# Kernel tuning notes

Measured on AMD Instinct MI355X. Metric: run time of the kernel, lower is better.

## Reference

```python
import jax, jax.numpy as jnp
import numpy as np

N = 100_000      # nodes (10kb Hi-C bins)
E = 3_200_000    # edges (avg degree 32)
IN = 6           # histone-mark features
HID1 = 6
HID2 = 30
HEADS = 4
NEG_SLOPE = 0.2  # PyG GATConv default LeakyReLU slope


def setup_inputs() -> dict:
    key = jax.random.key(0)
    ks = jax.random.split(key, 16)
    def glorot(k, shape, fan_in):
        return (jax.random.normal(k, shape, jnp.float32) / np.float32(np.sqrt(fan_in)))
    x = jax.random.normal(ks[0], (N, IN), jnp.float32)
    edge_index = jax.random.randint(ks[1], (2, E), 0, N, dtype=jnp.int32)
    edge_attr = jax.random.uniform(ks[2], (E,), jnp.float32)  # ignored (edge_dim=None)
    # GATConv 1: IN -> HID1, HEADS, concat=True
    w1 = glorot(ks[3], (IN, HEADS * HID1), IN)
    att_src1 = glorot(ks[4], (HEADS, HID1), HID1)
    att_dst1 = glorot(ks[5], (HEADS, HID1), HID1)
    b1 = jnp.zeros((HEADS * HID1,), jnp.float32)
    # GATConv 2: HEADS*HID1 -> HID2, HEADS, concat=False (head mean)
    w2 = glorot(ks[6], (HEADS * HID1, HEADS * HID2), HEADS * HID1)
    att_src2 = glorot(ks[7], (HEADS, HID2), HID2)
    att_dst2 = glorot(ks[8], (HEADS, HID2), HID2)
    b2 = jnp.zeros((HID2,), jnp.float32)
    # MLP head
    ffw1 = glorot(ks[9], (HID2, HID2 // 2), HID2)
    ffb1 = jnp.zeros((HID2 // 2,), jnp.float32)
    ffw2 = glorot(ks[10], (HID2 // 2, 2), HID2 // 2)
    ffb2 = jnp.zeros((2,), jnp.float32)
    return {"x": x, "edge_index": edge_index, "edge_attr": edge_attr,
            "w1": w1, "att_src1": att_src1, "att_dst1": att_dst1, "b1": b1,
            "w2": w2, "att_src2": att_src2, "att_dst2": att_dst2, "b2": b2,
            "ffw1": ffw1, "ffb1": ffb1, "ffw2": ffw2, "ffb2": ffb2}


def _leaky(z):
    return jnp.where(z > 0, z, NEG_SLOPE * z)


def _gat_conv(x, src, dst, W, a_src, a_dst, b, heads, ch, concat):
    n = x.shape[0]
    h = (x @ W).reshape(n, heads, ch)                       # [N,H,C]
    asrc = jnp.einsum('nhc,hc->nh', h, a_src)               # [N,H]
    adst = jnp.einsum('nhc,hc->nh', h, a_dst)               # [N,H]
    e = _leaky(asrc[src] + adst[dst])                       # [E,H]
    # stable segment softmax over incoming edges of each dst node
    m = jax.ops.segment_max(e, dst, num_segments=n)
    e = jnp.exp(e - m[dst])
    denom = jax.ops.segment_sum(e, dst, num_segments=n)
    alpha = e / (denom[dst] + 1e-16)                        # [E,H]
    msg = h[src] * alpha[:, :, None]                        # [E,H,C]
    out = jax.ops.segment_sum(msg, dst, num_segments=n)     # [N,H,C]
    out = out.reshape(n, heads * ch) if concat else out.mean(axis=1)
    return out + b


def reference(x, edge_index, edge_attr, w1, att_src1, att_dst1, b1,
              w2, att_src2, att_dst2, b2, ffw1, ffb1, ffw2, ffb2):
    n = x.shape[0]
    # PyG GATConv add_self_loops=True (edge_attr ignored: edge_dim=None)
    loops = jnp.arange(n, dtype=edge_index.dtype)
    ei = jnp.concatenate([edge_index, jnp.stack([loops, loops])], axis=1)
    src, dst = ei[0], ei[1]
    h = jax.nn.relu(_gat_conv(x, src, dst, w1, att_src1, att_dst1, b1, HEADS, HID1, True))
    h = jax.nn.relu(_gat_conv(h, src, dst, w2, att_src2, att_dst2, b2, HEADS, HID2, False))
    # dropout(p=0.5) is identity at inference
    h = jax.nn.relu(h @ ffw1 + ffb1)
    return h @ ffw2 + ffb2
```

## Files before the change

### kernel.cpp

```cpp
#include <hip/hip_runtime.h>
#include <hip/hip_fp16.h>

#define NEG_SLOPE 0.2f
#define NPB 128
#define MAXB 1024

__global__ void p0_count(const int* __restrict__ dst, int* __restrict__ bcnt,
                         int E, int nbuck)
{
    __shared__ int hist[MAXB];
    for (int b = threadIdx.x; b < nbuck; b += blockDim.x) hist[b] = 0;
    __syncthreads();
    int tile = blockIdx.x * 4096;
    int cnt = min(4096, E - tile);
    for (int k = threadIdx.x; k < cnt; k += blockDim.x)
        atomicAdd(&hist[dst[tile + k] >> 7], 1);
    __syncthreads();
    for (int b = threadIdx.x; b < nbuck; b += blockDim.x) {
        int v = hist[b];
        if (v) atomicAdd(&bcnt[b], v);
    }
}

__global__ void p1_scan(const int* __restrict__ bcnt, int* __restrict__ bbase,
                        int* __restrict__ bcur, int nbuck)
{
    __shared__ int sm[MAXB];
    int t = threadIdx.x;
    int v = (t < nbuck) ? bcnt[t] : 0;
    sm[t] = v;
    __syncthreads();
    for (int off = 1; off < MAXB; off <<= 1) {
        int x = (t >= off) ? sm[t - off] : 0;
        __syncthreads();
        sm[t] += x;
        __syncthreads();
    }
    if (t < nbuck) { int e = sm[t] - v; bbase[t] = e; bcur[t] = e; }
}

__global__ void p2_scatter(const int* __restrict__ src, const int* __restrict__ dst,
                           int* __restrict__ bcur, int* __restrict__ ebuf,
                           int E, int nbuck)
{
    __shared__ int hist[MAXB];
    __shared__ int base[MAXB];
    __shared__ int pk[4096];
    __shared__ unsigned short pb[4096];
    for (int b = threadIdx.x; b < nbuck; b += blockDim.x) hist[b] = 0;
    __syncthreads();
    int tile = blockIdx.x * 4096;
    int cnt = min(4096, E - tile);
    for (int k = threadIdx.x; k < cnt; k += blockDim.x) {
        int i = tile + k;
        int d = dst[i];
        int b = d >> 7;
        pk[k] = (src[i] << 7) | (d & 127);
        pb[k] = (unsigned short)b;
        atomicAdd(&hist[b], 1);
    }
    __syncthreads();
    for (int b = threadIdx.x; b < nbuck; b += blockDim.x) {
        int v = hist[b];
        base[b] = v ? atomicAdd(&bcur[b], v) : 0;
        hist[b] = 0;
    }
    __syncthreads();
    for (int k = threadIdx.x; k < cnt; k += blockDim.x) {
        int b = pb[k];
        int r = atomicAdd(&hist[b], 1);
        ebuf[base[b] + r] = pk[k];
    }
}

__global__ void p3_sort(const int* __restrict__ bbase, const int* __restrict__ bcnt,
                        const int* __restrict__ ebuf,
                        int* __restrict__ rowp, int* __restrict__ deg,
                        int* __restrict__ esrc, int N)
{
    __shared__ int hist[NPB];
    __shared__ int ls[NPB];
    int b = blockIdx.x;
    int n0 = b * NPB;
    if (threadIdx.x < NPB) hist[threadIdx.x] = 0;
    __syncthreads();
    int es = bbase[b], ec = bcnt[b];
    for (int k = threadIdx.x; k < ec; k += blockDim.x)
        atomicAdd(&hist[ebuf[es + k] & 127], 1);
    __syncthreads();
    if (threadIdx.x < NPB) ls[threadIdx.x] = hist[threadIdx.x];
    __syncthreads();
    for (int off = 1; off < NPB; off <<= 1) {
        int v = 0;
        if (threadIdx.x < NPB && threadIdx.x >= off) v = ls[threadIdx.x - off];
        __syncthreads();
        if (threadIdx.x < NPB) ls[threadIdx.x] += v;
        __syncthreads();
    }
    if (threadIdx.x < NPB) {
        int ex = ls[threadIdx.x] - hist[threadIdx.x];
        ls[threadIdx.x] = ex;
        int n = n0 + threadIdx.x;
        if (n < N) { rowp[n] = es + ex; deg[n] = hist[threadIdx.x]; }
        hist[threadIdx.x] = 0;
    }
    __syncthreads();
    for (int k = threadIdx.x; k < ec; k += blockDim.x) {
        int v = ebuf[es + k];
        int ln = v & 127;
        int r = atomicAdd(&hist[ln], 1);
        esrc[es + ls[ln] + r] = v >> 7;
    }
}

__global__ void k_fold(const float* __restrict__ W1,
                       const float* __restrict__ s1, const float* __restrict__ d1,
                       const float* __restrict__ W2,
                       const float* __restrict__ s2, const float* __restrict__ d2,
                       float* __restrict__ fold)
{
    int t = threadIdx.x;
    if (t < 24) {
        int h = t / 6, k = t % 6;
        float v = 0.f;
        for (int c = 0; c < 6; ++c) v += W1[k * 24 + h * 6 + c] * s1[h * 6 + c];
        fold[t] = v;
    } else if (t < 48) {
        int u = t - 24, h = u / 6, k = u % 6;
        float v = 0.f;
        for (int c = 0; c < 6; ++c) v += W1[k * 24 + h * 6 + c] * d1[h * 6 + c];
        fold[t] = v;
    } else if (t < 144) {
        int u = t - 48, h = u / 24, k = u % 24;
        float v = 0.f;
        for (int c = 0; c < 30; ++c) v += W2[k * 120 + h * 30 + c] * s2[h * 30 + c];
        fold[t] = v;
    } else if (t < 240) {
        int u = t - 144, h = u / 24, k = u % 24;
        float v = 0.f;
        for (int c = 0; c < 30; ++c) v += W2[k * 120 + h * 30 + c] * d2[h * 30 + c];
        fold[t] = v;
    }
}

__global__ void k1_logits(const float* __restrict__ x,
                          const float* __restrict__ fold,
                          float* __restrict__ as1, float* __restrict__ ad1, int N)
{
    int n = blockIdx.x * blockDim.x + threadIdx.x;
    if (n >= N) return;
    float xv[6];
#pragma unroll
    for (int k = 0; k < 6; ++k) xv[k] = x[n * 6 + k];
#pragma unroll
    for (int h = 0; h < 4; ++h) {
        float as = 0.f, ad = 0.f;
#pragma unroll
        for (int k = 0; k < 6; ++k) {
            as += xv[k] * fold[h * 6 + k];
            ad += xv[k] * fold[24 + h * 6 + k];
        }
        as1[n * 4 + h] = as;
        ad1[n * 4 + h] = ad;
    }
}

__global__ void k_gather1(const int* __restrict__ rowp, const int* __restrict__ deg,
                          const int* __restrict__ esrc,
                          const float* __restrict__ x,
                          const float* __restrict__ as1, const float* __restrict__ ad1,
                          const float* __restrict__ W1, const float* __restrict__ b1,
                          const float* __restrict__ fold,
                          __half* __restrict__ g1h,
                          float* __restrict__ as2, float* __restrict__ ad2, int N)
{
    int t = blockIdx.x * blockDim.x + threadIdx.x;
    int n = t >> 3;
    if (n >= N) return;
    int o = t & 7;
    int h = o & 3;
    int half = o >> 2;
    float adn = ad1[n * 4 + h];

    float acc[6] = {0.f, 0.f, 0.f, 0.f, 0.f, 0.f};
    float den = 0.f;
    if (half == 0) {
        float e0 = as1[n * 4 + h] + adn;
        e0 = e0 > 0.f ? e0 : NEG_SLOPE * e0;
        float w = expf(e0);
        den = w;
        const float2* xp = (const float2*)(x + (size_t)n * 6);
        float2 a = xp[0], b = xp[1], c = xp[2];
        acc[0] = w * a.x; acc[1] = w * a.y; acc[2] = w * b.x;
        acc[3] = w * b.y; acc[4] = w * c.x; acc[5] = w * c.y;
    }
    int start = rowp[n], cnt = deg[n];
    for (int k = half; k < cnt; k += 2) {
        int s = esrc[start + k];
        float e = as1[s * 4 + h] + adn;
        e = e > 0.f ? e : NEG_SLOPE * e;
        float w = expf(e);
        den += w;
        const float2* xp = (const float2*)(x + (size_t)s * 6);
        float2 a = xp[0], b = xp[1], c = xp[2];
        acc[0] += w * a.x; acc[1] += w * a.y; acc[2] += w * b.x;
        acc[3] += w * b.y; acc[4] += w * c.x; acc[5] += w * c.y;
    }
    den += __shfl_xor(den, 4);
#pragma unroll
    for (int k = 0; k < 6; ++k) acc[k] += __shfl_xor(acc[k], 4);

    float inv = 1.f / (den + 1e-16f);
    float m[6];
#pragma unroll
    for (int k = 0; k < 6; ++k) m[k] = acc[k] * inv;

    float gc[6];
#pragma unroll
    for (int c = 0; c < 6; ++c) {
        float v = b1[h * 6 + c];
#pragma unroll
        for (int k = 0; k < 6; ++k) v += m[k] * W1[k * 24 + h * 6 + c];
        gc[c] = v > 0.f ? v : 0.f;
    }
    float pas[4], pad[4];
#pragma unroll
    for (int hh = 0; hh < 4; ++hh) {
        float a = 0.f, d = 0.f;
#pragma unroll
        for (int c = 0; c < 6; ++c) {
            a += gc[c] * fold[48 + hh * 24 + h * 6 + c];
            d += gc[c] * fold[144 + hh * 24 + h * 6 + c];
        }
        pas[hh] = a; pad[hh] = d;
    }
#pragma unroll
    for (int hh = 0; hh < 4; ++hh) {
        pas[hh] += __shfl_xor(pas[hh], 1);
        pas[hh] += __shfl_xor(pas[hh], 2);
        pad[hh] += __shfl_xor(pad[hh], 1);
        pad[hh] += __shfl_xor(pad[hh], 2);
    }
    if (half == 0) {
        __half2 p0 = __floats2half2_rn(gc[0], gc[1]);
        __half2 p1 = __floats2half2_rn(gc[2], gc[3]);
        __half2 p2 = __floats2half2_rn(gc[4], gc[5]);
        unsigned int* gp = (unsigned int*)(g1h + (size_t)n * 24 + h * 6);
        gp[0] = *(unsigned int*)&p0;
        gp[1] = *(unsigned int*)&p1;
        gp[2] = *(unsigned int*)&p2;
        as2[n * 4 + h] = pas[h];
        ad2[n * 4 + h] = pad[h];
    }
}

__global__ void k_gather2(const int* __restrict__ rowp, const int* __restrict__ deg,
                          const int* __restrict__ esrc,
                          const __half* __restrict__ g1h,
                          const float* __restrict__ as2, const float* __restrict__ ad2,
                          const float* __restrict__ W2, const float* __restrict__ b2,
                          const float* __restrict__ fw1, const float* __restrict__ fb1,
                          const float* __restrict__ fw2, const float* __restrict__ fb2,
                          float* __restrict__ out, int N)
{
    int t = blockIdx.x * blockDim.x + threadIdx.x;
    int n = t >> 3;
    if (n >= N) return;
    int o = t & 7;
    int h = o & 3;
    int half = o >> 2;
    float adn = ad2[n * 4 + h];

    float acc[24];
#pragma unroll
    for (int k = 0; k < 24; ++k) acc[k] = 0.f;
    float den = 0.f;

    if (half == 0) {
        float e0 = as2[n * 4 + h] + adn;
        e0 = e0 > 0.f ? e0 : NEG_SLOPE * e0;
        float w = expf(e0);
        den = w;
        const uint4* gp = (const uint4*)(g1h + (size_t)n * 24);
#pragma unroll
        for (int q = 0; q < 3; ++q) {
            uint4 u = gp[q];
            float2 f0 = __half22float2(*(__half2*)&u.x);
            float2 f1 = __half22float2(*(__half2*)&u.y);
            float2 f2 = __half22float2(*(__half2*)&u.z);
            float2 f3 = __half22float2(*(__half2*)&u.w);
            acc[q * 8 + 0] = w * f0.x; acc[q * 8 + 1] = w * f0.y;
            acc[q * 8 + 2] = w * f1.x; acc[q * 8 + 3] = w * f1.y;
            acc[q * 8 + 4] = w * f2.x; acc[q * 8 + 5] = w * f2.y;
            acc[q * 8 + 6] = w * f3.x; acc[q * 8 + 7] = w * f3.y;
        }
    }
    int start = rowp[n], cnt = deg[n];
    for (int k = half; k < cnt; k += 2) {
        int s = esrc[start + k];
        float e = as2[s * 4 + h] + adn;
        e = e > 0.f ? e : NEG_SLOPE * e;
        float w = expf(e);
        den += w;
        const uint4* gp = (const uint4*)(g1h + (size_t)s * 24);
#pragma unroll
        for (int q = 0; q < 3; ++q) {
            uint4 u = gp[q];
            float2 f0 = __half22float2(*(__half2*)&u.x);
            float2 f1 = __half22float2(*(__half2*)&u.y);
            float2 f2 = __half22float2(*(__half2*)&u.z);
            float2 f3 = __half22float2(*(__half2*)&u.w);
            acc[q * 8 + 0] += w * f0.x; acc[q * 8 + 1] += w * f0.y;
            acc[q * 8 + 2] += w * f1.x; acc[q * 8 + 3] += w * f1.y;
            acc[q * 8 + 4] += w * f2.x; acc[q * 8 + 5] += w * f2.y;
            acc[q * 8 + 6] += w * f3.x; acc[q * 8 + 7] += w * f3.y;
        }
    }
    den += __shfl_xor(den, 4);
#pragma unroll
    for (int k = 0; k < 24; ++k) acc[k] += __shfl_xor(acc[k], 4);

    float inv = 1.f / (den + 1e-16f);
#pragma unroll
    for (int k = 0; k < 24; ++k) acc[k] *= inv;

    float zz[15];
#pragma unroll
    for (int cc = 0; cc < 15; ++cc) {
        int c = half * 15 + cc;
        float v = 0.f;
#pragma unroll
        for (int k = 0; k < 24; ++k) v += acc[k] * W2[k * 120 + h * 30 + c];
        v += __shfl_xor(v, 1);
        v += __shfl_xor(v, 2);
        zz[cc] = v;
    }
    float zhi[15];
#pragma unroll
    for (int cc = 0; cc < 15; ++cc) zhi[cc] = __shfl_xor(zz[cc], 4);

    if (o == 0) {
        float z[30];
#pragma unroll
        for (int cc = 0; cc < 15; ++cc) {
            float v0 = 0.25f * zz[cc] + b2[cc];
            float v1 = 0.25f * zhi[cc] + b2[15 + cc];
            z[cc]      = v0 > 0.f ? v0 : 0.f;
            z[15 + cc] = v1 > 0.f ? v1 : 0.f;
        }
        float m2[15];
#pragma unroll
        for (int j = 0; j < 15; ++j) {
            float v = fb1[j];
#pragma unroll
            for (int c = 0; c < 30; ++c) v += z[c] * fw1[c * 15 + j];
            m2[j] = v > 0.f ? v : 0.f;
        }
#pragma unroll
        for (int k = 0; k < 2; ++k) {
            float v = fb2[k];
#pragma unroll
            for (int j = 0; j < 15; ++j) v += m2[j] * fw2[j * 2 + k];
            out[(size_t)n * 2 + k] = v;
        }
    }
}

extern "C" void kernel_launch(void* const* d_in, const int* in_sizes, int n_in,
                              void* d_out, int out_size, void* d_ws, size_t ws_size,
                              hipStream_t stream)
{
    const float* x    = (const float*)d_in[0];
    const int*   ei   = (const int*)  d_in[1];
    const float* w1   = (const float*)d_in[3];
    const float* as1w = (const float*)d_in[4];
    const float* ad1w = (const float*)d_in[5];
    const float* b1   = (const float*)d_in[6];
    const float* w2   = (const float*)d_in[7];
    const float* as2w = (const float*)d_in[8];
    const float* ad2w = (const float*)d_in[9];
    const float* b2   = (const float*)d_in[10];
    const float* fw1  = (const float*)d_in[11];
    const float* fb1  = (const float*)d_in[12];
    const float* fw2  = (const float*)d_in[13];
    const float* fb2  = (const float*)d_in[14];

    const int N = in_sizes[0] / 6;
    const int E = in_sizes[1] / 2;
    const int* src = ei;
    const int* dst = ei + E;
    const int nbuck = (N + NPB - 1) / NPB;

    float* ws = (float*)d_ws;
    size_t off = 0;
    float* as1  = ws + off; off += (size_t)N * 4;
    float* ad1  = ws + off; off += (size_t)N * 4;
    float* as2  = ws + off; off += (size_t)N * 4;
    float* ad2  = ws + off; off += (size_t)N * 4;
    float* fold = ws + off; off += 256;
    __half* g1h = (__half*)(ws + off); off += (size_t)N * 12;

    int* iw = (int*)(ws + off);
    size_t ioff = 0;
    int* bcnt  = iw + ioff; ioff += MAXB;
    int* bbase = iw + ioff; ioff += MAXB;
    int* bcur  = iw + ioff; ioff += MAXB;
    int* rowp  = iw + ioff; ioff += N;
    int* deg   = iw + ioff; ioff += N;
    int* ebuf  = iw + ioff; ioff += E;
    int* esrc  = iw + ioff; ioff += E;

    hipMemsetAsync(bcnt, 0, MAXB * sizeof(int), stream);

    const int B = 256;
    const int NB = (N + B - 1) / B;
    const int TB = (E + 4095) / 4096;
    const int OB = ((size_t)N * 8 + B - 1) / B;

    k_fold    <<<1, 256, 0, stream>>>(w1, as1w, ad1w, w2, as2w, ad2w, fold);

    p0_count  <<<TB, B, 0, stream>>>(dst, bcnt, E, nbuck);
    p1_scan   <<<1, MAXB, 0, stream>>>(bcnt, bbase, bcur, nbuck);
    p2_scatter<<<TB, B, 0, stream>>>(src, dst, bcur, ebuf, E, nbuck);
    p3_sort   <<<nbuck, B, 0, stream>>>(bbase, bcnt, ebuf, rowp, deg, esrc, N);

    k1_logits <<<NB, B, 0, stream>>>(x, fold, as1, ad1, N);
    k_gather1 <<<OB, B, 0, stream>>>(rowp, deg, esrc, x, as1, ad1, w1, b1,
                                     fold, g1h, as2, ad2, N);

    k_gather2 <<<OB, B, 0, stream>>>(rowp, deg, esrc, g1h, as2, ad2, w2, b2,
                                     fw1, fb1, fw2, fb2, (float*)d_out, N);
}
```

Baseline: 377.6 us.

## Pack per-node gather rows into 32-byte records and split layer-2 gather in halves

Layer-1 source logits (fp16) and features are packed into one 32-byte row per node so each edge gather touches a single aligned record. Layer-2 features plus fp16 source logits are split into two 32-byte row arrays, and the second gather is split into two kernels, each covering 12 input channels, with a partial z buffer between them. The aim is to shrink each kernel's random-access working set so it fits in cache better and to cut register pressure. In exchange the edge list is traversed one extra time, attention weights are recomputed in both kernels, a 30-float-per-node intermediate is added, and source logits are stored at fp16 precision.

```diff
diff --git a/kernel.cpp b/kernel.cpp
--- a/kernel.cpp
+++ b/kernel.cpp
@@ -4,6 +4,15 @@
 #define NEG_SLOPE 0.2f
 #define NPB 128
 #define MAXB 1024
+
+__device__ __forceinline__ unsigned pk2(float a, float b) {
+    __half2 h = __floats2half2_rn(a, b);
+    return *(unsigned*)&h;
+}
+__device__ __forceinline__ float exh(unsigned u, int hi) {
+    __half2 h = *(__half2*)&u;
+    return hi ? __high2float(h) : __low2float(h);
+}
 
 __global__ void p0_count(const int* __restrict__ dst, int* __restrict__ bcnt,
                          int E, int nbuck)
@@ -143,36 +152,48 @@
     }
 }
 
-__global__ void k1_logits(const float* __restrict__ x,
-                          const float* __restrict__ fold,
-                          float* __restrict__ as1, float* __restrict__ ad1, int N)
+__global__ void k1_row(const float* __restrict__ x,
+                       const float* __restrict__ fold,
+                       float* __restrict__ row1, float* __restrict__ ad1, int N)
 {
     int n = blockIdx.x * blockDim.x + threadIdx.x;
     if (n >= N) return;
     float xv[6];
 #pragma unroll
     for (int k = 0; k < 6; ++k) xv[k] = x[n * 6 + k];
+    float as[4], ad[4];
 #pragma unroll
     for (int h = 0; h < 4; ++h) {
-        float as = 0.f, ad = 0.f;
+        float a = 0.f, d = 0.f;
 #pragma unroll
         for (int k = 0; k < 6; ++k) {
-            as += xv[k] * fold[h * 6 + k];
-            ad += xv[k] * fold[24 + h * 6 + k];
+            a += xv[k] * fold[h * 6 + k];
+            d += xv[k] * fold[24 + h * 6 + k];
         }
-        as1[n * 4 + h] = as;
-        ad1[n * 4 + h] = ad;
-    }
+        as[h] = a; ad[h] = d;
+        ad1[n * 4 + h] = d;
+    }
+    uint4 u0, u1;
+    u0.x = pk2(as[0], as[1]);
+    u0.y = pk2(as[2], as[3]);
+    u0.z = __float_as_uint(xv[0]);
+    u0.w = __float_as_uint(xv[1]);
+    u1.x = __float_as_uint(xv[2]);
+    u1.y = __float_as_uint(xv[3]);
+    u1.z = __float_as_uint(xv[4]);
+    u1.w = __float_as_uint(xv[5]);
+    uint4* rp = (uint4*)row1 + (size_t)n * 2;
+    rp[0] = u0; rp[1] = u1;
 }
 
 __global__ void k_gather1(const int* __restrict__ rowp, const int* __restrict__ deg,
                           const int* __restrict__ esrc,
-                          const float* __restrict__ x,
-                          const float* __restrict__ as1, const float* __restrict__ ad1,
+                          const float* __restrict__ row1,
+                          const float* __restrict__ ad1,
                           const float* __restrict__ W1, const float* __restrict__ b1,
                           const float* __restrict__ fold,
-                          __half* __restrict__ g1h,
-                          float* __restrict__ as2, float* __restrict__ ad2, int N)
+                          float* __restrict__ rowA, float* __restrict__ rowB,
+                          float* __restrict__ ad2, int N)
 {
     int t = blockIdx.x * blockDim.x + threadIdx.x;
     int n = t >> 3;
@@ -181,30 +202,39 @@
     int h = o & 3;
     int half = o >> 2;
     float adn = ad1[n * 4 + h];
+    const uint4* R = (const uint4*)row1;
 
     float acc[6] = {0.f, 0.f, 0.f, 0.f, 0.f, 0.f};
     float den = 0.f;
     if (half == 0) {
-        float e0 = as1[n * 4 + h] + adn;
+        uint4 u0 = R[(size_t)n * 2], u1 = R[(size_t)n * 2 + 1];
+        float asn = exh((h < 2) ? u0.x : u0.y, h & 1);
+        float e0 = asn + adn;
         e0 = e0 > 0.f ? e0 : NEG_SLOPE * e0;
         float w = expf(e0);
         den = w;
-        const float2* xp = (const float2*)(x + (size_t)n * 6);
-        float2 a = xp[0], b = xp[1], c = xp[2];
-        acc[0] = w * a.x; acc[1] = w * a.y; acc[2] = w * b.x;
-        acc[3] = w * b.y; acc[4] = w * c.x; acc[5] = w * c.y;
+        acc[0] = w * __uint_as_float(u0.z);
+        acc[1] = w * __uint_as_float(u0.w);
+        acc[2] = w * __uint_as_float(u1.x);
+        acc[3] = w * __uint_as_float(u1.y);
+        acc[4] = w * __uint_as_float(u1.z);
+        acc[5] = w * __uint_as_float(u1.w);
     }
     int start = rowp[n], cnt = deg[n];
     for (int k = half; k < cnt; k += 2) {
         int s = esrc[start + k];
-        float e = as1[s * 4 + h] + adn;
+        uint4 u0 = R[(size_t)s * 2], u1 = R[(size_t)s * 2 + 1];
+        float as = exh((h < 2) ? u0.x : u0.y, h & 1);
+        float e = as + adn;
         e = e > 0.f ? e : NEG_SLOPE * e;
         float w = expf(e);
         den += w;
-        const float2* xp = (const float2*)(x + (size_t)s * 6);
-        float2 a = xp[0], b = xp[1], c = xp[2];
-        acc[0] += w * a.x; acc[1] += w * a.y; acc[2] += w * b.x;
-        acc[3] += w * b.y; acc[4] += w * c.x; acc[5] += w * c.y;
+        acc[0] += w * __uint_as_float(u0.z);
+        acc[1] += w * __uint_as_float(u0.w);
+        acc[2] += w * __uint_as_float(u1.x);
+        acc[3] += w * __uint_as_float(u1.y);
+        acc[4] += w * __uint_as_float(u1.z);
+        acc[5] += w * __uint_as_float(u1.w);
     }
     den += __shfl_xor(den, 4);
 #pragma unroll
@@ -242,26 +272,24 @@
         pad[hh] += __shfl_xor(pad[hh], 2);
     }
     if (half == 0) {
-        __half2 p0 = __floats2half2_rn(gc[0], gc[1]);
-        __half2 p1 = __floats2half2_rn(gc[2], gc[3]);
-        __half2 p2 = __floats2half2_rn(gc[4], gc[5]);
-        unsigned int* gp = (unsigned int*)(g1h + (size_t)n * 24 + h * 6);
-        gp[0] = *(unsigned int*)&p0;
-        gp[1] = *(unsigned int*)&p1;
-        gp[2] = *(unsigned int*)&p2;
-        as2[n * 4 + h] = pas[h];
+        unsigned* rp = (unsigned*)((h < 2) ? rowA : rowB) + (size_t)n * 8;
+        if ((h & 1) == 0) {
+            rp[0] = pk2(pas[0], pas[1]);
+            rp[1] = pk2(pas[2], pas[3]);
+        }
+        int gb = 2 + (h & 1) * 3;
+        rp[gb + 0] = pk2(gc[0], gc[1]);
+        rp[gb + 1] = pk2(gc[2], gc[3]);
+        rp[gb + 2] = pk2(gc[4], gc[5]);
         ad2[n * 4 + h] = pad[h];
     }
 }
 
-__global__ void k_gather2(const int* __restrict__ rowp, const int* __restrict__ deg,
-                          const int* __restrict__ esrc,
-                          const __half* __restrict__ g1h,
-                          const float* __restrict__ as2, const float* __restrict__ ad2,
-                          const float* __restrict__ W2, const float* __restrict__ b2,
-                          const float* __restrict__ fw1, const float* __restrict__ fb1,
-                          const float* __restrict__ fw2, const float* __restrict__ fb2,
-                          float* __restrict__ out, int N)
+__global__ void k_g2a(const int* __restrict__ rowp, const int* __restrict__ deg,
+                      const int* __restrict__ esrc,
+                      const float* __restrict__ rowA, const float* __restrict__ ad2,
+                      const float* __restrict__ W2,
+                      float* __restrict__ zA, int N)
 {
     int t = blockIdx.x * blockDim.x + threadIdx.x;
     int n = t >> 3;
@@ -270,67 +298,143 @@
     int h = o & 3;
     int half = o >> 2;
     float adn = ad2[n * 4 + h];
-
-    float acc[24];
-#pragma unroll
-    for (int k = 0; k < 24; ++k) acc[k] = 0.f;
+    const uint4* R = (const uint4*)rowA;
+
+    float acc[12];
+#pragma unroll
+    for (int k = 0; k < 12; ++k) acc[k] = 0.f;
     float den = 0.f;
 
     if (half == 0) {
-        float e0 = as2[n * 4 + h] + adn;
-        e0 = e0 > 0.f ? e0 : NEG_SLOPE * e0;
-        float w = expf(e0);
+        uint4 u0 = R[(size_t)n * 2], u1 = R[(size_t)n * 2 + 1];
+        float as = exh((h < 2) ? u0.x : u0.y, h & 1);
+        float e = as + adn; e = e > 0.f ? e : NEG_SLOPE * e;
+        float w = expf(e);
         den = w;
-        const uint4* gp = (const uint4*)(g1h + (size_t)n * 24);
-#pragma unroll
-        for (int q = 0; q < 3; ++q) {
-            uint4 u = gp[q];
-            float2 f0 = __half22float2(*(__half2*)&u.x);
-            float2 f1 = __half22float2(*(__half2*)&u.y);
-            float2 f2 = __half22float2(*(__half2*)&u.z);
-            float2 f3 = __half22float2(*(__half2*)&u.w);
-            acc[q * 8 + 0] = w * f0.x; acc[q * 8 + 1] = w * f0.y;
-            acc[q * 8 + 2] = w * f1.x; acc[q * 8 + 3] = w * f1.y;
-            acc[q * 8 + 4] = w * f2.x; acc[q * 8 + 5] = w * f2.y;
-            acc[q * 8 + 6] = w * f3.x; acc[q * 8 + 7] = w * f3.y;
-        }
+        float2 g0 = __half22float2(*(__half2*)&u0.z);
+        float2 g1 = __half22float2(*(__half2*)&u0.w);
+        float2 g2 = __half22float2(*(__half2*)&u1.x);
+        float2 g3 = __half22float2(*(__half2*)&u1.y);
+        float2 g4 = __half22float2(*(__half2*)&u1.z);
+        float2 g5 = __half22float2(*(__half2*)&u1.w);
+        acc[0]=w*g0.x; acc[1]=w*g0.y; acc[2]=w*g1.x; acc[3]=w*g1.y;
+        acc[4]=w*g2.x; acc[5]=w*g2.y; acc[6]=w*g3.x; acc[7]=w*g3.y;
+        acc[8]=w*g4.x; acc[9]=w*g4.y; acc[10]=w*g5.x; acc[11]=w*g5.y;
     }
     int start = rowp[n], cnt = deg[n];
     for (int k = half; k < cnt; k += 2) {
         int s = esrc[start + k];
-        float e = as2[s * 4 + h] + adn;
-        e = e > 0.f ? e : NEG_SLOPE * e;
+        uint4 u0 = R[(size_t)s * 2], u1 = R[(size_t)s * 2 + 1];
+        float as = exh((h < 2) ? u0.x : u0.y, h & 1);
+        float e = as + adn; e = e > 0.f ? e : NEG_SLOPE * e;
         float w = expf(e);
         den += w;
-        const uint4* gp = (const uint4*)(g1h + (size_t)s * 24);
-#pragma unroll
-        for (int q = 0; q < 3; ++q) {
-            uint4 u = gp[q];
-            float2 f0 = __half22float2(*(__half2*)&u.x);
-            float2 f1 = __half22float2(*(__half2*)&u.y);
-            float2 f2 = __half22float2(*(__half2*)&u.z);
-            float2 f3 = __half22float2(*(__half2*)&u.w);
-            acc[q * 8 + 0] += w * f0.x; acc[q * 8 + 1] += w * f0.y;
-            acc[q * 8 + 2] += w * f1.x; acc[q * 8 + 3] += w * f1.y;
-            acc[q * 8 + 4] += w * f2.x; acc[q * 8 + 5] += w * f2.y;
-            acc[q * 8 + 6] += w * f3.x; acc[q * 8 + 7] += w * f3.y;
-        }
+        float2 g0 = __half22float2(*(__half2*)&u0.z);
+        float2 g1 = __half22float2(*(__half2*)&u0.w);
+        float2 g2 = __half22float2(*(__half2*)&u1.x);
+        float2 g3 = __half22float2(*(__half2*)&u1.y);
+        float2 g4 = __half22float2(*(__half2*)&u1.z);
+        float2 g5 = __half22float2(*(__half2*)&u1.w);
+        acc[0]+=w*g0.x; acc[1]+=w*g0.y; acc[2]+=w*g1.x; acc[3]+=w*g1.y;
+        acc[4]+=w*g2.x; acc[5]+=w*g2.y; acc[6]+=w*g3.x; acc[7]+=w*g3.y;
+        acc[8]+=w*g4.x; acc[9]+=w*g4.y; acc[10]+=w*g5.x; acc[11]+=w*g5.y;
     }
     den += __shfl_xor(den, 4);
 #pragma unroll
-    for (int k = 0; k < 24; ++k) acc[k] += __shfl_xor(acc[k], 4);
-
+    for (int k = 0; k < 12; ++k) acc[k] += __shfl_xor(acc[k], 4);
     float inv = 1.f / (den + 1e-16f);
 #pragma unroll
-    for (int k = 0; k < 24; ++k) acc[k] *= inv;
-
-    float zz[15];
+    for (int k = 0; k < 12; ++k) acc[k] *= inv;
+
+    float vv[15];
 #pragma unroll
     for (int cc = 0; cc < 15; ++cc) {
         int c = half * 15 + cc;
         float v = 0.f;
 #pragma unroll
-        for (int k = 0; k < 24; ++k) v += acc[k] * W2[k * 120 + h * 30 + c];
+        for (int k = 0; k < 12; ++k) v += acc[k] * W2[k * 120 + h * 30 + c];
+        v += __shfl_xor(v, 1);
+        v += __shfl_xor(v, 2);
+        vv[cc] = v;
+    }
+    if (h == 0) {
+#pragma unroll
+        for (int cc = 0; cc < 15; ++cc)
+            zA[(size_t)n * 30 + half * 15 + cc] = vv[cc];
+    }
+}
+
+__global__ void k_g2b(const int* __restrict__ rowp, const int* __restrict__ deg,
+                      const int* __restrict__ esrc,
+                      const float* __restrict__ rowB, const float* __restrict__ ad2,
+                      const float* __restrict__ W2, const float* __restrict__ zA,
+                      const float* __restrict__ b2,
+                      const float* __restrict__ fw1, const float* __restrict__ fb1,
+                      const float* __restrict__ fw2, const float* __restrict__ fb2,
+                      float* __restrict__ out, int N)
+{
+    int t = blockIdx.x * blockDim.x + threadIdx.x;
+    int n = t >> 3;
+    if (n >= N) return;
+    int o = t & 7;
+    int h = o & 3;
+    int half = o >> 2;
+    float adn = ad2[n * 4 + h];
+    const uint4* R = (const uint4*)rowB;
+
+    float acc[12];
+#pragma unroll
+    for (int k = 0; k < 12; ++k) acc[k] = 0.f;
+    float den = 0.f;
+
+    if (half == 0) {
+        uint4 u0 = R[(size_t)n * 2], u1 = R[(size_t)n * 2 + 1];
+        float as = exh((h < 2) ? u0.x : u0.y, h & 1);
+        float e = as + adn; e = e > 0.f ? e : NEG_SLOPE * e;
+        float w = expf(e);
+        den = w;
+        float2 g0 = __half22float2(*(__half2*)&u0.z);
+        float2 g1 = __half22float2(*(__half2*)&u0.w);
+        float2 g2 = __half22float2(*(__half2*)&u1.x);
+        float2 g3 = __half22float2(*(__half2*)&u1.y);
+        float2 g4 = __half22float2(*(__half2*)&u1.z);
+        float2 g5 = __half22float2(*(__half2*)&u1.w);
+        acc[0]=w*g0.x; acc[1]=w*g0.y; acc[2]=w*g1.x; acc[3]=w*g1.y;
+        acc[4]=w*g2.x; acc[5]=w*g2.y; acc[6]=w*g3.x; acc[7]=w*g3.y;
+        acc[8]=w*g4.x; acc[9]=w*g4.y; acc[10]=w*g5.x; acc[11]=w*g5.y;
+    }
+    int start = rowp[n], cnt = deg[n];
+    for (int k = half; k < cnt; k += 2) {
+        int s = esrc[start + k];
+        uint4 u0 = R[(size_t)s * 2], u1 = R[(size_t)s * 2 + 1];
+        float as = exh((h < 2) ? u0.x : u0.y, h & 1);
+        float e = as + adn; e = e > 0.f ? e : NEG_SLOPE * e;
+        float w = expf(e);
+        den += w;
+        float2 g0 = __half22float2(*(__half2*)&u0.z);
+        float2 g1 = __half22float2(*(__half2*)&u0.w);
+        float2 g2 = __half22float2(*(__half2*)&u1.x);
+        float2 g3 = __half22float2(*(__half2*)&u1.y);
+        float2 g4 = __half22float2(*(__half2*)&u1.z);
+        float2 g5 = __half22float2(*(__half2*)&u1.w);
+        acc[0]+=w*g0.x; acc[1]+=w*g0.y; acc[2]+=w*g1.x; acc[3]+=w*g1.y;
+        acc[4]+=w*g2.x; acc[5]+=w*g2.y; acc[6]+=w*g3.x; acc[7]+=w*g3.y;
+        acc[8]+=w*g4.x; acc[9]+=w*g4.y; acc[10]+=w*g5.x; acc[11]+=w*g5.y;
+    }
+    den += __shfl_xor(den, 4);
+#pragma unroll
+    for (int k = 0; k < 12; ++k) acc[k] += __shfl_xor(acc[k], 4);
+    float inv = 1.f / (den + 1e-16f);
+#pragma unroll
+    for (int k = 0; k < 12; ++k) acc[k] *= inv;
+
+    float zz[15];
+#pragma unroll
+    for (int cc = 0; cc < 15; ++cc) {
+        int c = half * 15 + cc;
+        float v = 0.f;
+#pragma unroll
+        for (int k = 0; k < 12; ++k) v += acc[k] * W2[(12 + k) * 120 + h * 30 + c];
         v += __shfl_xor(v, 1);
         v += __shfl_xor(v, 2);
         zz[cc] = v;
@@ -343,8 +447,8 @@
         float z[30];
 #pragma unroll
         for (int cc = 0; cc < 15; ++cc) {
-            float v0 = 0.25f * zz[cc] + b2[cc];
-            float v1 = 0.25f * zhi[cc] + b2[15 + cc];
+            float v0 = 0.25f * (zz[cc] + zA[(size_t)n * 30 + cc]) + b2[cc];
+            float v1 = 0.25f * (zhi[cc] + zA[(size_t)n * 30 + 15 + cc]) + b2[15 + cc];
             z[cc]      = v0 > 0.f ? v0 : 0.f;
             z[15 + cc] = v1 > 0.f ? v1 : 0.f;
         }
@@ -393,12 +497,13 @@
 
     float* ws = (float*)d_ws;
     size_t off = 0;
-    float* as1  = ws + off; off += (size_t)N * 4;
+    float* row1 = ws + off; off += (size_t)N * 8;
+    float* rowA = ws + off; off += (size_t)N * 8;
+    float* rowB = ws + off; off += (size_t)N * 8;
     float* ad1  = ws + off; off += (size_t)N * 4;
-    float* as2  = ws + off; off += (size_t)N * 4;
     float* ad2  = ws + off; off += (size_t)N * 4;
+    float* zA   = ws + off; off += (size_t)N * 30;
     float* fold = ws + off; off += 256;
-    __half* g1h = (__half*)(ws + off); off += (size_t)N * 12;
 
     int* iw = (int*)(ws + off);
     size_t ioff = 0;
@@ -424,10 +529,11 @@
     p2_scatter<<<TB, B, 0, stream>>>(src, dst, bcur, ebuf, E, nbuck);
     p3_sort   <<<nbuck, B, 0, stream>>>(bbase, bcnt, ebuf, rowp, deg, esrc, N);
 
-    k1_logits <<<NB, B, 0, stream>>>(x, fold, as1, ad1, N);
-    k_gather1 <<<OB, B, 0, stream>>>(rowp, deg, esrc, x, as1, ad1, w1, b1,
-                                     fold, g1h, as2, ad2, N);
-
-    k_gather2 <<<OB, B, 0, stream>>>(rowp, deg, esrc, g1h, as2, ad2, w2, b2,
+    k1_row    <<<NB, B, 0, stream>>>(x, fold, row1, ad1, N);
+    k_gather1 <<<OB, B, 0, stream>>>(rowp, deg, esrc, row1, ad1, w1, b1, fold,
+                                     rowA, rowB, ad2, N);
+
+    k_g2a     <<<OB, B, 0, stream>>>(rowp, deg, esrc, rowA, ad2, w2, zA, N);
+    k_g2b     <<<OB, B, 0, stream>>>(rowp, deg, esrc, rowB, ad2, w2, zA, b2,
                                      fw1, fb1, fw2, fb2, (float*)d_out, N);
 }
```

Result: slower. 395.2 us (+4.7%).
